# Kernel optimization log

Hardware: AMD Instinct MI355X
Metric: run time of the kernel (lower is better)

The kernel has to match this reference:

```python
import jax, jax.numpy as jnp
import numpy as np

UNITS = 512
MEMORY_SIZE = 16


def setup_inputs() -> dict:
    key = jax.random.key(0)
    k1, k2, k3, k4, k5 = jax.random.split(key, 5)
    B, T, D = 256, 128, 512
    inputs = jax.random.normal(k1, (B, T, D), dtype=jnp.float32)
    dones = jax.random.randint(k2, (B, T), 0, 2, dtype=jnp.int32)
    state = jnp.zeros((B, UNITS), dtype=jnp.float32)
    step = jnp.zeros((B, 1), dtype=jnp.int32)
    # GRU params (Keras default reset_after=True: dual bias [2, 3*units])
    W = jax.random.normal(k3, (D, 3 * UNITS), dtype=jnp.float32) * 0.05
    U = jax.random.normal(k4, (UNITS, 3 * UNITS), dtype=jnp.float32) * 0.05
    b = jax.random.normal(k5, (2, 3 * UNITS), dtype=jnp.float32) * 0.05
    return {"inputs": inputs, "dones": dones, "state": state, "step": step,
            "W": W, "U": U, "b": b}


def _gru_cell(h, x, W, U, b):
    # Keras GRU, reset_after=True
    xm = x @ W + b[0]          # [B, 3U]
    hm = h @ U + b[1]          # [B, 3U]
    xz, xr, xh = jnp.split(xm, 3, axis=-1)
    hz, hr, hh = jnp.split(hm, 3, axis=-1)
    z = jax.nn.sigmoid(xz + hz)
    r = jax.nn.sigmoid(xr + hr)
    hcand = jnp.tanh(xh + r * hh)
    return z * h + (1.0 - z) * hcand


def reference(inputs, dones, state, step, W, U, b):
    # inputs: [B, T, D]; dones: [B, T]; state: [B, U]; step: [B, 1] int32
    x_t = jnp.transpose(inputs, (1, 0, 2))  # [T, B, D]
    d_t = jnp.transpose(dones, (1, 0))      # [T, B]

    def scan_fn(carry, xs):
        h, s = carry
        x, d = xs
        h_new = _gru_cell(h, x, W, U, b)
        s_new = s + 1
        reset = (d == 1) | ((s_new[:, 0] % MEMORY_SIZE) == 0)  # [B]
        h_out = jnp.where(reset[:, None], 0.0, h_new)
        s_out = jnp.where(reset[:, None], 0, s_new)
        # hidden_state emitted per step is the cell output BEFORE reset masking
        return (h_out, s_out), h_new

    (state_f, step_f), seq = jax.lax.scan(scan_fn, (state, step), (x_t, d_t))
    sequences = jnp.transpose(seq, (1, 0, 2))  # [B, T, U]
    return sequences, state_f, step_f
```

## Files before the change

### kernel.cpp

```cpp
#include <hip/hip_runtime.h>
#include <cstdint>

#define UNITS 512
#define NB 256
#define NT 128
#define ND 512
#define G3 1536

#define SEQ_ELEMS (16777216L)
#define STATE_OFF (SEQ_ELEMS)
#define STEP_OFF  (SEQ_ELEMS + 131072L)

#define BGS 16
#define ROWS_PER_BG 16

#define WS_FLAG_OFF 4096
#define WS_H_OFF    65536
#define H_ELEMS     131072L

typedef unsigned short u16;
typedef short short8 __attribute__((ext_vector_type(8)));
typedef float f32x4 __attribute__((ext_vector_type(4)));

__device__ __forceinline__ u16 f2b(float f) {
  unsigned int x = __float_as_uint(f);
  unsigned int r = (x + 0x7FFFu + ((x >> 16) & 1u)) >> 16;
  return (u16)r;
}
__device__ __forceinline__ float b2f(u16 u) {
  return __uint_as_float(((unsigned int)u) << 16);
}

template<int MODE>
__device__ __forceinline__ float ldf(const void* p, long idx) {
  if (MODE) return b2f(((const u16*)p)[idx]);
  else      return ((const float*)p)[idx];
}

__device__ __forceinline__ void store_h_coherent(const u16* p, u16 v) {
  unsigned int vv = v;
  asm volatile("global_store_short %0, %1, off sc0 sc1"
               :: "v"(p), "v"(vv) : "memory");
}
__device__ __forceinline__ void store_flag_coherent(const unsigned int* p, unsigned int v) {
  asm volatile("global_store_dword %0, %1, off sc0 sc1"
               :: "v"(p), "v"(v) : "memory");
}
__device__ __forceinline__ unsigned int load_flag_coherent(const unsigned int* p) {
  unsigned int v;
  asm volatile("global_load_dword %0, %1, off sc0 sc1\n\t"
               "s_waitcnt vmcnt(0)"
               : "=v"(v) : "v"(p) : "memory");
  return v;
}

__device__ __forceinline__ void load_h16_coherent(const u16* p, short8 hf[16]) {
  asm volatile(
    "global_load_dwordx4 %0, %16, off sc0 sc1\n\t"
    "global_load_dwordx4 %1, %16, off offset:64 sc0 sc1\n\t"
    "global_load_dwordx4 %2, %16, off offset:128 sc0 sc1\n\t"
    "global_load_dwordx4 %3, %16, off offset:192 sc0 sc1\n\t"
    "global_load_dwordx4 %4, %16, off offset:256 sc0 sc1\n\t"
    "global_load_dwordx4 %5, %16, off offset:320 sc0 sc1\n\t"
    "global_load_dwordx4 %6, %16, off offset:384 sc0 sc1\n\t"
    "global_load_dwordx4 %7, %16, off offset:448 sc0 sc1\n\t"
    "global_load_dwordx4 %8, %16, off offset:512 sc0 sc1\n\t"
    "global_load_dwordx4 %9, %16, off offset:576 sc0 sc1\n\t"
    "global_load_dwordx4 %10, %16, off offset:640 sc0 sc1\n\t"
    "global_load_dwordx4 %11, %16, off offset:704 sc0 sc1\n\t"
    "global_load_dwordx4 %12, %16, off offset:768 sc0 sc1\n\t"
    "global_load_dwordx4 %13, %16, off offset:832 sc0 sc1\n\t"
    "global_load_dwordx4 %14, %16, off offset:896 sc0 sc1\n\t"
    "global_load_dwordx4 %15, %16, off offset:960 sc0 sc1\n\t"
    "s_waitcnt vmcnt(0)"
    : "=&v"(hf[0]), "=&v"(hf[1]), "=&v"(hf[2]), "=&v"(hf[3]),
      "=&v"(hf[4]), "=&v"(hf[5]), "=&v"(hf[6]), "=&v"(hf[7]),
      "=&v"(hf[8]), "=&v"(hf[9]), "=&v"(hf[10]), "=&v"(hf[11]),
      "=&v"(hf[12]), "=&v"(hf[13]), "=&v"(hf[14]), "=&v"(hf[15])
    : "v"(p)
    : "memory");
}

__global__ void sniff_init(const void* W, unsigned int* wsu) {
  int l = threadIdx.x;
  unsigned int v = ((const unsigned int*)W)[l];
  unsigned int elo = (v >> 7) & 0xFFu;
  bool inband = (elo > 90u) && (elo < 130u);
  unsigned long long m = __ballot(inband);
  int cnt = __popcll(m);
  if (l == 0) wsu[0] = (cnt >= 32) ? 1u : 0u;
}

__global__ void h_init(const void* state, void* ws) {
  unsigned int flag = *(const unsigned int*)ws;
  u16* h0 = (u16*)((char*)ws + WS_H_OFF);
  int i = blockIdx.x * blockDim.x + threadIdx.x;
  if (i < (int)H_ELEMS) {
    h0[i] = flag ? ((const u16*)state)[i] : f2b(((const float*)state)[i]);
  }
  if (i < 4096) {
    ((unsigned int*)((char*)ws + WS_FLAG_OFF))[i] = 0u;
  }
}

template<int MODE>
__device__ void stage_cols(const void* M, int ug, u16* lds) {
  int tid = threadIdx.x;
  #pragma unroll 4
  for (int it = 0; it < 192; ++it) {
    int idx = it * 256 + tid;
    int k = idx / 96;
    int c = idx - k * 96;
    int col = (c >> 5) * UNITS + ug * 32 + (c & 31);
    float v = ldf<MODE>(M, (long)k * G3 + col);
    unsigned int byte = (unsigned int)c * 1024u +
                        ((((unsigned int)k) * 2u) ^ (((unsigned int)(c & 7)) << 4));
    *(u16*)((char*)lds + byte) = f2b(v);
  }
}

__device__ __forceinline__ short8 read_bfrag(const u16* lds, int c, int k) {
  unsigned int byte = (unsigned int)c * 1024u +
                      ((((unsigned int)k) * 2u) ^ (((unsigned int)(c & 7)) << 4));
  return *(const short8*)((const char*)lds + byte);
}

#define MFMA(a, b, c) __builtin_amdgcn_mfma_f32_16x16x32_bf16((a), (b), (c), 0, 0, 0)

template<int MODE>
__global__ __launch_bounds__(256, 1)
void gru_run(const void* __restrict__ xin, const int* __restrict__ dones,
             const int* __restrict__ stepin, const void* __restrict__ stin,
             const void* __restrict__ W,
             const void* __restrict__ U, const void* __restrict__ bias,
             void* __restrict__ out, void* __restrict__ ws)
{
  unsigned int flag = *(const unsigned int*)ws;
  if (flag != (unsigned int)MODE) return;

  __shared__ u16 wl[96 * 512];
  __shared__ float xmbuf[2][2][3][64][4];
  __shared__ unsigned int sv[8];

  const int tid  = threadIdx.x;
  const int wv   = tid >> 6;
  const int l    = tid & 63;
  const int l15  = l & 15;
  const int ksub = (l >> 4) * 8;
  const int rsub = (l >> 4) * 4;

  const int bg = blockIdx.x & 15;
  const int ug = blockIdx.x >> 4;
  const int r0 = bg * ROWS_PER_BG;

  unsigned int* flags = (unsigned int*)((char*)ws + WS_FLAG_OFF);
  u16* hws = (u16*)((char*)ws + WS_H_OFF);

  if (tid < 8) sv[tid] = 0u;

  stage_cols<MODE>(U, ug, wl);
  __syncthreads();
  short8 ufz[16], ufrr[16], ufh[16];
  if (wv < 2) {
    #pragma unroll
    for (int kt = 0; kt < 16; ++kt) {
      int kb = kt * 32 + ksub;
      ufz[kt]  = read_bfrag(wl,      wv * 16 + l15, kb);
      ufrr[kt] = read_bfrag(wl, 32 + wv * 16 + l15, kb);
      ufh[kt]  = read_bfrag(wl, 64 + wv * 16 + l15, kb);
    }
  }
  __syncthreads();
  stage_cols<MODE>(W, ug, wl);
  __syncthreads();

  if (wv >= 2) {
    const int xw = wv - 2;
    const int c0 = xw * 16 + l15, c1 = 32 + xw * 16 + l15, c2 = 64 + xw * 16 + l15;
    for (int t = 0; t < NT; ++t) {
      const int p = t & 1;
      long xbase = ((long)(r0 + l15) * NT + t) * ND + ksub;
      short8 xf[16];
      #pragma unroll
      for (int kt = 0; kt < 16; ++kt) {
        if (MODE) {
          xf[kt] = *(const short8*)((const u16*)xin + xbase + kt * 32);
        } else {
          const float* q = (const float*)xin + xbase + kt * 32;
          f32x4 lo = *(const f32x4*)q;
          f32x4 hi = *(const f32x4*)(q + 4);
          short8 r;
          r[0] = (short)f2b(lo[0]); r[1] = (short)f2b(lo[1]);
          r[2] = (short)f2b(lo[2]); r[3] = (short)f2b(lo[3]);
          r[4] = (short)f2b(hi[0]); r[5] = (short)f2b(hi[1]);
          r[6] = (short)f2b(hi[2]); r[7] = (short)f2b(hi[3]);
          xf[kt] = r;
        }
      }
      if (t >= 2) {
        unsigned int tgt = 2u * (unsigned int)(t >> 1);
        while (__hip_atomic_load(&sv[2 + p], __ATOMIC_ACQUIRE,
                                 __HIP_MEMORY_SCOPE_WORKGROUP) < tgt) {}
      }
      f32x4 az = {0,0,0,0}, ar = {0,0,0,0}, axh = {0,0,0,0};
      #pragma unroll
      for (int kt = 0; kt < 16; ++kt) {
        int kb = kt * 32 + ksub;
        az  = MFMA(xf[kt], read_bfrag(wl, c0, kb), az);
        ar  = MFMA(xf[kt], read_bfrag(wl, c1, kb), ar);
        axh = MFMA(xf[kt], read_bfrag(wl, c2, kb), axh);
      }
      *(f32x4*)&xmbuf[p][xw][0][l][0] = az;
      *(f32x4*)&xmbuf[p][xw][1][l][0] = ar;
      *(f32x4*)&xmbuf[p][xw][2][l][0] = axh;
      if (l == 0)
        __hip_atomic_fetch_add(&sv[p], 1u, __ATOMIC_RELEASE,
                               __HIP_MEMORY_SCOPE_WORKGROUP);
    }
    return;
  }

  const int w = wv;
  const int j = ug * 32 + w * 16 + l15;

  float bzs = ldf<MODE>(bias, j)        + ldf<MODE>(bias, G3 + j);
  float brs = ldf<MODE>(bias, 512 + j)  + ldf<MODE>(bias, G3 + 512 + j);
  float bxh = ldf<MODE>(bias, 1024 + j);
  float bhh = ldf<MODE>(bias, (long)G3 + 1024 + j);

  int sarr[4];
  float hprev[4];
  #pragma unroll
  for (int i = 0; i < 4; ++i) {
    int row = r0 + rsub + i;
    sarr[i]  = stepin[row];
    hprev[i] = ldf<MODE>(stin, (long)row * UNITS + j);
  }

  for (int t = 0; t < NT; ++t) {
    const int p = t & 1;
    int d4_[4];
    #pragma unroll
    for (int i = 0; i < 4; ++i) d4_[i] = dones[(long)(r0 + rsub + i) * NT + t];

    if (t > 0) {
      const unsigned int* myf = flags + (long)(bg * 16 + l15) * 16;
      bool pred;
      do {
        unsigned int fv = (l < 16) ? load_flag_coherent(myf) : (unsigned int)t;
        pred = (fv >= (unsigned int)t);
      } while (!__all(pred));
    }

    const u16* hb = hws + p * H_ELEMS;
    long hbase = (long)(r0 + l15) * UNITS + ksub;
    short8 hf[16];
    load_h16_coherent(hb + hbase, hf);

    {
      unsigned int tgt = 2u * (unsigned int)((t >> 1) + 1);
      while (__hip_atomic_load(&sv[p], __ATOMIC_ACQUIRE,
                               __HIP_MEMORY_SCOPE_WORKGROUP) < tgt) {}
    }
    f32x4 az  = *(const f32x4*)&xmbuf[p][w][0][l][0];
    f32x4 ar  = *(const f32x4*)&xmbuf[p][w][1][l][0];
    f32x4 axh = *(const f32x4*)&xmbuf[p][w][2][l][0];
    f32x4 ahh = {0,0,0,0};

    #pragma unroll
    for (int kt = 0; kt < 16; ++kt) {
      az  = MFMA(hf[kt], ufz[kt],  az);
      ar  = MFMA(hf[kt], ufrr[kt], ar);
      ahh = MFMA(hf[kt], ufh[kt],  ahh);
    }
    if (l == 0)
      __hip_atomic_fetch_add(&sv[2 + p], 1u, __ATOMIC_RELEASE,
                             __HIP_MEMORY_SCOPE_WORKGROUP);

    u16* hn = hws + (p ^ 1) * H_ELEMS;
    float hnew_r[4];
    #pragma unroll
    for (int i = 0; i < 4; ++i) {
      int row = r0 + rsub + i;
      float z  = 1.0f / (1.0f + __expf(-(az[i] + bzs)));
      float rr = 1.0f / (1.0f + __expf(-(ar[i] + brs)));
      float tx = axh[i] + bxh + rr * (ahh[i] + bhh);
      tx = fminf(15.0f, fmaxf(-15.0f, tx));
      float e  = __expf(2.0f * tx);
      float hcand = (e - 1.0f) / (e + 1.0f);
      float hnew = z * hprev[i] + (1.0f - z) * hcand;
      hnew_r[i] = hnew;

      int sn = sarr[i] + 1;
      bool reset = (d4_[i] == 1) || ((sn & 15) == 0);
      float hkeep = reset ? 0.0f : hnew;
      sarr[i] = reset ? 0 : sn;
      hprev[i] = hkeep;
      store_h_coherent(hn + (long)row * UNITS + j, f2b(hkeep));
    }

    if (t < NT - 1) {
      asm volatile("s_waitcnt vmcnt(0)" ::: "memory");
      unsigned int old = 0;
      if (l == 0)
        old = __hip_atomic_fetch_add(&sv[4], 1u, __ATOMIC_ACQ_REL,
                                     __HIP_MEMORY_SCOPE_WORKGROUP);
      if (l == 0 && old == 2u * (unsigned int)t + 1u)
        store_flag_coherent(flags + (long)(bg * 16 + ug) * 16,
                            (unsigned int)t + 1u);
    }

    #pragma unroll
    for (int i = 0; i < 4; ++i) {
      int row = r0 + rsub + i;
      long qo = ((long)row * NT + t) * UNITS + j;
      if (MODE) ((u16*)out)[qo] = f2b(hnew_r[i]);
      else      ((float*)out)[qo] = hnew_r[i];

      if (t == NT - 1) {
        long so = STATE_OFF + (long)row * UNITS + j;
        if (MODE) ((u16*)out)[so] = f2b(hprev[i]);
        else      ((float*)out)[so] = hprev[i];
        if (w == 0 && l15 == 0 && ug == 0) {
          long po = STEP_OFF + row;
          float sval = (float)sarr[i];
          if (MODE) ((u16*)out)[po] = f2b(sval);
          else      ((float*)out)[po] = sval;
        }
      }
    }
  }
}

extern "C" void kernel_launch(void* const* d_in, const int* in_sizes, int n_in,
                              void* d_out, int out_size, void* d_ws, size_t ws_size,
                              hipStream_t stream) {
  const void* xin    = d_in[0];
  const int*  dones  = (const int*)d_in[1];
  const void* stin   = d_in[2];
  const int*  stepin = (const int*)d_in[3];
  const void* W      = d_in[4];
  const void* U      = d_in[5];
  const void* bias   = d_in[6];

  sniff_init<<<1, 64, 0, stream>>>(W, (unsigned int*)d_ws);
  h_init<<<256, 512, 0, stream>>>(stin, d_ws);
  gru_run<0><<<256, 256, 0, stream>>>(xin, dones, stepin, stin, W, U, bias, d_out, d_ws);
  gru_run<1><<<256, 256, 0, stream>>>(xin, dones, stepin, stin, W, U, bias, d_out, d_ws);
}
```

Measured before the change: 725.7 us.

## Replace per-step flag polling with sentinel-valued hidden state in a 4-deep ring

```diff
diff --git a/kernel.cpp b/kernel.cpp
--- a/kernel.cpp
+++ b/kernel.cpp
@@ -14,21 +14,21 @@
 #define BGS 16
 #define ROWS_PER_BG 16
 
-#define WS_FLAG_OFF 4096
 #define WS_H_OFF    65536
 #define H_ELEMS     131072L
 
 typedef unsigned short u16;
 typedef short short8 __attribute__((ext_vector_type(8)));
 typedef float f32x4 __attribute__((ext_vector_type(4)));
+typedef unsigned int u32;
 
 __device__ __forceinline__ u16 f2b(float f) {
-  unsigned int x = __float_as_uint(f);
-  unsigned int r = (x + 0x7FFFu + ((x >> 16) & 1u)) >> 16;
+  u32 x = __float_as_uint(f);
+  u32 r = (x + 0x7FFFu + ((x >> 16) & 1u)) >> 16;
   return (u16)r;
 }
 __device__ __forceinline__ float b2f(u16 u) {
-  return __uint_as_float(((unsigned int)u) << 16);
+  return __uint_as_float(((u32)u) << 16);
 }
 
 template<int MODE>
@@ -38,20 +38,15 @@
 }
 
 __device__ __forceinline__ void store_h_coherent(const u16* p, u16 v) {
-  unsigned int vv = v;
+  u32 vv = v;
   asm volatile("global_store_short %0, %1, off sc0 sc1"
                :: "v"(p), "v"(vv) : "memory");
 }
-__device__ __forceinline__ void store_flag_coherent(const unsigned int* p, unsigned int v) {
-  asm volatile("global_store_dword %0, %1, off sc0 sc1"
-               :: "v"(p), "v"(v) : "memory");
-}
-__device__ __forceinline__ unsigned int load_flag_coherent(const unsigned int* p) {
-  unsigned int v;
-  asm volatile("global_load_dword %0, %1, off sc0 sc1\n\t"
-               "s_waitcnt vmcnt(0)"
-               : "=v"(v) : "v"(p) : "memory");
-  return v;
+__device__ __forceinline__ void store_sent16(const u16* p) {
+  f32x4 s;
+  s[0] = __uint_as_float(0xFFFFFFFFu); s[1] = s[0]; s[2] = s[0]; s[3] = s[0];
+  asm volatile("global_store_dwordx4 %0, %1, off sc0 sc1"
+               :: "v"(p), "v"(s) : "memory");
 }
 
 __device__ __forceinline__ void load_h16_coherent(const u16* p, short8 hf[16]) {
@@ -81,10 +76,16 @@
     : "memory");
 }
 
-__global__ void sniff_init(const void* W, unsigned int* wsu) {
+__device__ __forceinline__ u32 pkmax(u32 a, u32 b) {
+  u32 r;
+  asm("v_pk_max_u16 %0, %1, %2" : "=v"(r) : "v"(a), "v"(b));
+  return r;
+}
+
+__global__ void sniff_init(const void* W, u32* wsu) {
   int l = threadIdx.x;
-  unsigned int v = ((const unsigned int*)W)[l];
-  unsigned int elo = (v >> 7) & 0xFFu;
+  u32 v = ((const u32*)W)[l];
+  u32 elo = (v >> 7) & 0xFFu;
   bool inband = (elo > 90u) && (elo < 130u);
   unsigned long long m = __ballot(inband);
   int cnt = __popcll(m);
@@ -92,14 +93,14 @@
 }
 
 __global__ void h_init(const void* state, void* ws) {
-  unsigned int flag = *(const unsigned int*)ws;
+  u32 flag = *(const u32*)ws;
   u16* h0 = (u16*)((char*)ws + WS_H_OFF);
   int i = blockIdx.x * blockDim.x + threadIdx.x;
   if (i < (int)H_ELEMS) {
     h0[i] = flag ? ((const u16*)state)[i] : f2b(((const float*)state)[i]);
-  }
-  if (i < 4096) {
-    ((unsigned int*)((char*)ws + WS_FLAG_OFF))[i] = 0u;
+    h0[i + H_ELEMS]     = 0xFFFFu;
+    h0[i + 2 * H_ELEMS] = 0xFFFFu;
+    h0[i + 3 * H_ELEMS] = 0xFFFFu;
   }
 }
 
@@ -113,15 +114,15 @@
     int c = idx - k * 96;
     int col = (c >> 5) * UNITS + ug * 32 + (c & 31);
     float v = ldf<MODE>(M, (long)k * G3 + col);
-    unsigned int byte = (unsigned int)c * 1024u +
-                        ((((unsigned int)k) * 2u) ^ (((unsigned int)(c & 7)) << 4));
+    u32 byte = (u32)c * 1024u +
+               ((((u32)k) * 2u) ^ (((u32)(c & 7)) << 4));
     *(u16*)((char*)lds + byte) = f2b(v);
   }
 }
 
 __device__ __forceinline__ short8 read_bfrag(const u16* lds, int c, int k) {
-  unsigned int byte = (unsigned int)c * 1024u +
-                      ((((unsigned int)k) * 2u) ^ (((unsigned int)(c & 7)) << 4));
+  u32 byte = (u32)c * 1024u +
+             ((((u32)k) * 2u) ^ (((u32)(c & 7)) << 4));
   return *(const short8*)((const char*)lds + byte);
 }
 
@@ -135,12 +136,13 @@
              const void* __restrict__ U, const void* __restrict__ bias,
              void* __restrict__ out, void* __restrict__ ws)
 {
-  unsigned int flag = *(const unsigned int*)ws;
-  if (flag != (unsigned int)MODE) return;
+  u32 flag = *(const u32*)ws;
+  if (flag != (u32)MODE) return;
 
   __shared__ u16 wl[96 * 512];
-  __shared__ float xmbuf[2][2][3][64][4];
-  __shared__ unsigned int sv[8];
+  __shared__ float xmbuf[4][2][3][64][4];
+  __shared__ int   dlds[16][NT];
+  __shared__ u32   sv[8];
 
   const int tid  = threadIdx.x;
   const int wv   = tid >> 6;
@@ -153,10 +155,14 @@
   const int ug = blockIdx.x >> 4;
   const int r0 = bg * ROWS_PER_BG;
 
-  unsigned int* flags = (unsigned int*)((char*)ws + WS_FLAG_OFF);
   u16* hws = (u16*)((char*)ws + WS_H_OFF);
 
   if (tid < 8) sv[tid] = 0u;
+  #pragma unroll
+  for (int q = 0; q < 8; ++q) {
+    int idx = q * 256 + tid;
+    dlds[idx >> 7][idx & 127] = dones[(long)(r0 + (idx >> 7)) * NT + (idx & 127)];
+  }
 
   stage_cols<MODE>(U, ug, wl);
   __syncthreads();
@@ -178,7 +184,8 @@
     const int xw = wv - 2;
     const int c0 = xw * 16 + l15, c1 = 32 + xw * 16 + l15, c2 = 64 + xw * 16 + l15;
     for (int t = 0; t < NT; ++t) {
-      const int p = t & 1;
+      const int p = t & 3;
+      const u32 u = (u32)(t >> 2);
       long xbase = ((long)(r0 + l15) * NT + t) * ND + ksub;
       short8 xf[16];
       #pragma unroll
@@ -197,10 +204,9 @@
           xf[kt] = r;
         }
       }
-      if (t >= 2) {
-        unsigned int tgt = 2u * (unsigned int)(t >> 1);
-        while (__hip_atomic_load(&sv[2 + p], __ATOMIC_ACQUIRE,
-                                 __HIP_MEMORY_SCOPE_WORKGROUP) < tgt) {}
+      if (u > 0) {
+        while (__hip_atomic_load(&sv[4 + p], __ATOMIC_ACQUIRE,
+                                 __HIP_MEMORY_SCOPE_WORKGROUP) < 2u * u) {}
       }
       f32x4 az = {0,0,0,0}, ar = {0,0,0,0}, axh = {0,0,0,0};
       #pragma unroll
@@ -213,9 +219,8 @@
       *(f32x4*)&xmbuf[p][xw][0][l][0] = az;
       *(f32x4*)&xmbuf[p][xw][1][l][0] = ar;
       *(f32x4*)&xmbuf[p][xw][2][l][0] = axh;
-      if (l == 0)
-        __hip_atomic_fetch_add(&sv[p], 1u, __ATOMIC_RELEASE,
-                               __HIP_MEMORY_SCOPE_WORKGROUP);
+      __hip_atomic_fetch_add(&sv[p], (l == 0) ? 1u : 0u, __ATOMIC_RELEASE,
+                             __HIP_MEMORY_SCOPE_WORKGROUP);
     }
     return;
   }
@@ -237,47 +242,49 @@
     hprev[i] = ldf<MODE>(stin, (long)row * UNITS + j);
   }
 
+  const long hbase = (long)(r0 + l15) * UNITS + ksub;
+
   for (int t = 0; t < NT; ++t) {
-    const int p = t & 1;
-    int d4_[4];
-    #pragma unroll
-    for (int i = 0; i < 4; ++i) d4_[i] = dones[(long)(r0 + rsub + i) * NT + t];
-
-    if (t > 0) {
-      const unsigned int* myf = flags + (long)(bg * 16 + l15) * 16;
-      bool pred;
-      do {
-        unsigned int fv = (l < 16) ? load_flag_coherent(myf) : (unsigned int)t;
-        pred = (fv >= (unsigned int)t);
-      } while (!__all(pred));
-    }
-
-    const u16* hb = hws + p * H_ELEMS;
-    long hbase = (long)(r0 + l15) * UNITS + ksub;
+    const int p = t & 3;
+    const u32 u = (u32)(t >> 2);
+
+    const u16* hg = hws + (long)(t & 3) * H_ELEMS;
     short8 hf[16];
-    load_h16_coherent(hb + hbase, hf);
-
-    {
-      unsigned int tgt = 2u * (unsigned int)((t >> 1) + 1);
-      while (__hip_atomic_load(&sv[p], __ATOMIC_ACQUIRE,
-                               __HIP_MEMORY_SCOPE_WORKGROUP) < tgt) {}
-    }
-    f32x4 az  = *(const f32x4*)&xmbuf[p][w][0][l][0];
-    f32x4 ar  = *(const f32x4*)&xmbuf[p][w][1][l][0];
-    f32x4 axh = *(const f32x4*)&xmbuf[p][w][2][l][0];
-    f32x4 ahh = {0,0,0,0};
-
+    for (;;) {
+      load_h16_coherent(hg + hbase, hf);
+      u32 m0 = 0, m1 = 0, m2 = 0, m3 = 0;
+      #pragma unroll
+      for (int kt = 0; kt < 16; ++kt) {
+        const u32* d = (const u32*)&hf[kt];
+        m0 = pkmax(m0, d[0]); m1 = pkmax(m1, d[1]);
+        m2 = pkmax(m2, d[2]); m3 = pkmax(m3, d[3]);
+      }
+      u32 m = pkmax(pkmax(m0, m1), pkmax(m2, m3));
+      bool ok = ((m & 0xFFFFu) != 0xFFFFu) && ((m >> 16) != 0xFFFFu);
+      if (__all(ok)) break;
+    }
+
+    f32x4 az = {0,0,0,0}, ar = {0,0,0,0}, ahh = {0,0,0,0};
     #pragma unroll
     for (int kt = 0; kt < 16; ++kt) {
       az  = MFMA(hf[kt], ufz[kt],  az);
       ar  = MFMA(hf[kt], ufrr[kt], ar);
       ahh = MFMA(hf[kt], ufh[kt],  ahh);
     }
-    if (l == 0)
-      __hip_atomic_fetch_add(&sv[2 + p], 1u, __ATOMIC_RELEASE,
-                             __HIP_MEMORY_SCOPE_WORKGROUP);
-
-    u16* hn = hws + (p ^ 1) * H_ELEMS;
+
+    while (__hip_atomic_load(&sv[p], __ATOMIC_ACQUIRE,
+                             __HIP_MEMORY_SCOPE_WORKGROUP) < 2u * (u + 1u)) {}
+    f32x4 axh = *(const f32x4*)&xmbuf[p][w][2][l][0];
+    {
+      f32x4 xz = *(const f32x4*)&xmbuf[p][w][0][l][0];
+      f32x4 xr = *(const f32x4*)&xmbuf[p][w][1][l][0];
+      az[0] += xz[0]; az[1] += xz[1]; az[2] += xz[2]; az[3] += xz[3];
+      ar[0] += xr[0]; ar[1] += xr[1]; ar[2] += xr[2]; ar[3] += xr[3];
+    }
+    __hip_atomic_fetch_add(&sv[4 + p], (l == 0) ? 1u : 0u, __ATOMIC_RELEASE,
+                           __HIP_MEMORY_SCOPE_WORKGROUP);
+
+    u16* hn = hws + (long)((t + 1) & 3) * H_ELEMS;
     float hnew_r[4];
     #pragma unroll
     for (int i = 0; i < 4; ++i) {
@@ -292,22 +299,21 @@
       hnew_r[i] = hnew;
 
       int sn = sarr[i] + 1;
-      bool reset = (d4_[i] == 1) || ((sn & 15) == 0);
+      bool reset = (dlds[rsub + i][t] == 1) || ((sn & 15) == 0);
       float hkeep = reset ? 0.0f : hnew;
       sarr[i] = reset ? 0 : sn;
       hprev[i] = hkeep;
-      store_h_coherent(hn + (long)row * UNITS + j, f2b(hkeep));
-    }
-
-    if (t < NT - 1) {
-      asm volatile("s_waitcnt vmcnt(0)" ::: "memory");
-      unsigned int old = 0;
-      if (l == 0)
-        old = __hip_atomic_fetch_add(&sv[4], 1u, __ATOMIC_ACQ_REL,
-                                     __HIP_MEMORY_SCOPE_WORKGROUP);
-      if (l == 0 && old == 2u * (unsigned int)t + 1u)
-        store_flag_coherent(flags + (long)(bg * 16 + ug) * 16,
-                            (unsigned int)t + 1u);
+      if (t < NT - 1)
+        store_h_coherent(hn + (long)row * UNITS + j, f2b(hkeep));
+    }
+
+    if (ug == 0 && t >= 1 && t < NT - 1) {
+      u16* inv = hws + (long)((t - 1) & 3) * H_ELEMS;
+      int irow = r0 + w * 8 + (l >> 3);
+      long ib = (long)irow * UNITS + (l & 7) * 8;
+      #pragma unroll
+      for (int q = 0; q < 8; ++q)
+        store_sent16(inv + ib + q * 64);
     }
 
     #pragma unroll
@@ -343,7 +349,7 @@
   const void* U      = d_in[5];
   const void* bias   = d_in[6];
 
-  sniff_init<<<1, 64, 0, stream>>>(W, (unsigned int*)d_ws);
+  sniff_init<<<1, 64, 0, stream>>>(W, (u32*)d_ws);
   h_init<<<256, 512, 0, stream>>>(stin, d_ws);
   gru_run<0><<<256, 256, 0, stream>>>(xin, dones, stepin, stin, W, U, bias, d_out, d_ws);
   gru_run<1><<<256, 256, 0, stream>>>(xin, dones, stepin, stin, W, U, bias, d_out, d_ws);
```

After: 1.146 ms. 1.58x slower.
